# Optimization experiments

Hardware: AMD Instinct MI355X
Metric: run time of the kernel (lower is better)

Reference implementation:

```python
import jax, jax.numpy as jnp
import numpy as np

B, N, D = 8, 4096, 256
H = 8
DH = D // H          # 32 per-head dim
M = 256              # number of random features
DEPTH = 4
HID = 4 * D          # mlp hidden
EPS = 1e-6


def layernorm(x, g, b):
    mu = jnp.mean(x, axis=-1, keepdims=True)
    var = jnp.mean(jnp.square(x - mu), axis=-1, keepdims=True)
    return (x - mu) * jax.lax.rsqrt(var + EPS) * g + b


def _phi(t, proj, is_query):
    # t: (B,H,N,DH), proj: (M,DH) -> (B,H,N,M) nonnegative softmax-kernel features
    nrm = DH ** -0.25
    td = t * nrm
    u = jnp.einsum('bhnd,md->bhnm', td, proj)
    diag = 0.5 * jnp.sum(td * td, axis=-1, keepdims=True)
    if is_query:
        mx = jnp.max(u, axis=-1, keepdims=True)
    else:
        mx = jnp.max(u, axis=(-2, -1), keepdims=True)
    return (jnp.exp(u - diag - mx) + 1e-4) / jnp.sqrt(jnp.asarray(M, t.dtype))


def performer_attn(h, Wqkv, Wproj, bproj, proj):
    # h: (B,N,D)
    qkv = h @ Wqkv                                   # (B,N,3D)
    q, k, v = jnp.split(qkv, 3, axis=-1)
    to_heads = lambda t: t.reshape(B, N, H, DH).transpose(0, 2, 1, 3)
    q, k, v = to_heads(q), to_heads(k), to_heads(v)  # (B,H,N,DH)
    qp = _phi(q, proj, True)                         # (B,H,N,M)
    kp = _phi(k, proj, False)                        # (B,H,N,M)
    kv = jnp.einsum('bhnm,bhnd->bhmd', kp, v)        # (B,H,M,DH) linear-time context
    z = 1.0 / (jnp.einsum('bhnm,bhm->bhn', qp, kp.sum(axis=2)) + 1e-6)
    out = jnp.einsum('bhnm,bhmd->bhnd', qp, kv) * z[..., None]
    out = out.transpose(0, 2, 1, 3).reshape(B, N, D)
    return out @ Wproj + bproj


def mlp(h, W1, b1, W2, b2):
    return jax.nn.gelu(h @ W1 + b1, approximate=False) @ W2 + b2


def setup_inputs() -> dict:
    key = jax.random.key(0)
    ks = jax.random.split(key, 10)
    inp = {
        'x': jax.random.normal(ks[0], (B, N, D), jnp.float32),
        'pos_emb': 0.02 * jax.random.normal(ks[1], (N, D), jnp.float32),
        'g1n': jnp.ones((D,), jnp.float32),
        'b1n': jnp.zeros((D,), jnp.float32),
        'g2n': jnp.ones((D,), jnp.float32),
        'b2n': jnp.zeros((D,), jnp.float32),
        'Wqkv': 0.02 * jax.random.normal(ks[2], (DEPTH, D, 3 * D), jnp.float32),
        'Wproj': 0.02 * jax.random.normal(ks[3], (DEPTH, D, D), jnp.float32),
        'bproj': jnp.zeros((DEPTH, D), jnp.float32),
        'W1': 0.02 * jax.random.normal(ks[4], (DEPTH, D, HID), jnp.float32),
        'b1m': jnp.zeros((DEPTH, HID), jnp.float32),
        'W2': 0.02 * jax.random.normal(ks[5], (DEPTH, HID, D), jnp.float32),
        'b2m': jnp.zeros((DEPTH, D), jnp.float32),
        'proj_mat': jax.random.normal(ks[6], (DEPTH, M, DH), jnp.float32),
    }
    return inp


def reference(x, pos_emb, g1n, b1n, g2n, b2n, Wqkv, Wproj, bproj, W1, b1m, W2, b2m, proj_mat):
    h = x + pos_emb[None]
    for l in range(DEPTH):  # small fixed depth
        h = h + performer_attn(layernorm(h, g1n, b1n), Wqkv[l], Wproj[l], bproj[l], proj_mat[l])
        h = h + mlp(layernorm(h, g2n, b2n), W1[l], b1m[l], W2[l], b2m[l])
    return h
```

## Files before the change

### kernel.cpp

```cpp
#include <hip/hip_runtime.h>
#include <hip/hip_bf16.h>
#include <math.h>

#define B 8
#define N 4096
#define D 256
#define H 8
#define DH 32
#define M 256
#define DEPTH 4
#define HID 1024
#define NRM 0.4204482076268573f

typedef __attribute__((ext_vector_type(8))) short short8;
typedef __attribute__((ext_vector_type(4))) float f32x4;

static __device__ __forceinline__ unsigned short f2bf(float f) {
    __hip_bfloat16 h = __float2bfloat16(f);
    return __builtin_bit_cast(unsigned short, h);
}
static __device__ __forceinline__ float bfu2f(unsigned short u) {
    unsigned int x = ((unsigned int)u) << 16;
    return __builtin_bit_cast(float, x);
}

__global__ void add_pos_kernel(const float* __restrict__ x, const float* __restrict__ pos,
                               float* __restrict__ h) {
    int i = blockIdx.x * 256 + threadIdx.x;
    int nd = i % (N * D);
    h[i] = x[i] + pos[nd];
}

__global__ void projbf_kernel(const float* __restrict__ in, unsigned short* __restrict__ out) {
    int i = blockIdx.x * 256 + threadIdx.x;
    out[i] = f2bf(in[i]);
}

__global__ __launch_bounds__(256) void wtrans_kernel(const float* __restrict__ in,
                                                     unsigned short* __restrict__ out,
                                                     int Kd, int Nd, int slim) {
    __shared__ float tl[32][33];
    int n0 = blockIdx.x * 32, k0 = blockIdx.y * 32;
    int t = threadIdx.x;
    int kk = t >> 3, c4 = (t & 7) * 4;
    float4 v = *reinterpret_cast<const float4*>(&in[(size_t)(k0 + kk) * Nd + n0 + c4]);
    tl[kk][c4 + 0] = v.x; tl[kk][c4 + 1] = v.y; tl[kk][c4 + 2] = v.z; tl[kk][c4 + 3] = v.w;
    __syncthreads();
    int nn = t >> 3, k4 = (t & 7) * 4;
    float sc = (n0 + nn < slim) ? NRM : 1.0f;
    ushort4 o;
    o.x = f2bf(tl[k4 + 0][nn] * sc); o.y = f2bf(tl[k4 + 1][nn] * sc);
    o.z = f2bf(tl[k4 + 2][nn] * sc); o.w = f2bf(tl[k4 + 3][nn] * sc);
    *reinterpret_cast<ushort4*>(&out[(size_t)(n0 + nn) * Kd + k0 + k4]) = o;
}

__global__ __launch_bounds__(256) void ln_kernel(const float* __restrict__ in,
                                                 const float* __restrict__ g,
                                                 const float* __restrict__ bb,
                                                 unsigned short* __restrict__ out) {
    int wave = threadIdx.x >> 6, lane = threadIdx.x & 63;
    long row = (long)blockIdx.x * 4 + wave;
    float4 v = reinterpret_cast<const float4*>(in + row * D)[lane];
    float s = v.x + v.y + v.z + v.w;
#pragma unroll
    for (int o = 32; o >= 1; o >>= 1) s += __shfl_xor(s, o);
    float mu = s * (1.0f / D);
    float d0 = v.x - mu, d1 = v.y - mu, d2 = v.z - mu, d3 = v.w - mu;
    float ss = d0 * d0 + d1 * d1 + d2 * d2 + d3 * d3;
#pragma unroll
    for (int o = 32; o >= 1; o >>= 1) ss += __shfl_xor(ss, o);
    float inv = rsqrtf(ss * (1.0f / D) + 1e-6f);
    float4 gv = reinterpret_cast<const float4*>(g)[lane];
    float4 bv = reinterpret_cast<const float4*>(bb)[lane];
    ushort4 o4;
    o4.x = f2bf(d0 * inv * gv.x + bv.x);
    o4.y = f2bf(d1 * inv * gv.y + bv.y);
    o4.z = f2bf(d2 * inv * gv.z + bv.z);
    o4.w = f2bf(d3 * inv * gv.w + bv.w);
    *reinterpret_cast<ushort4*>(&out[row * D + lane * 4]) = o4;
}

template <bool BIAS, bool GELU_ACT, bool RESID, bool OUT16>
__global__ __launch_bounds__(256) void mgemm_kernel(const unsigned short* __restrict__ A,
                                                    const unsigned short* __restrict__ Bt,
                                                    const float* __restrict__ bias,
                                                    float* __restrict__ C,
                                                    unsigned short* __restrict__ O16,
                                                    int K, int Nc) {
    __shared__ short Als[128][40];
    __shared__ short Bls[128][40];
    int t = threadIdx.x;
    int l = t & 63, w = t >> 6;
    int wr = w >> 1, wc = w & 1;
    int nwg = gridDim.x * gridDim.y;
    int bid = blockIdx.y * gridDim.x + blockIdx.x;
    int lgid = (bid & 7) * (nwg >> 3) + (bid >> 3);
    int bx = lgid % gridDim.x;
    int by = lgid / gridDim.x;
    long m0 = (long)by * 128;
    int n0 = bx * 128;
    int lr = l & 15;
    int lg = l >> 4;
    int kp8 = lg * 8;
    int srow = t >> 2, skoff = (t & 3) * 8;

    const unsigned short* Ap0 = &A[(size_t)(m0 + srow) * K + skoff];
    const unsigned short* Ap1 = Ap0 + (size_t)64 * K;
    const unsigned short* Bp0 = &Bt[(size_t)(n0 + srow) * K + skoff];
    const unsigned short* Bp1 = Bp0 + (size_t)64 * K;

    short8 ra0 = *reinterpret_cast<const short8*>(Ap0);
    short8 ra1 = *reinterpret_cast<const short8*>(Ap1);
    short8 rb0 = *reinterpret_cast<const short8*>(Bp0);
    short8 rb1 = *reinterpret_cast<const short8*>(Bp1);

    f32x4 acc[4][4];
#pragma unroll
    for (int i = 0; i < 4; i++)
#pragma unroll
        for (int j = 0; j < 4; j++) acc[i][j] = (f32x4){0.f, 0.f, 0.f, 0.f};

    for (int k0 = 0; k0 < K; k0 += 32) {
        *reinterpret_cast<short8*>(&Als[srow][skoff]) = ra0;
        *reinterpret_cast<short8*>(&Als[srow + 64][skoff]) = ra1;
        *reinterpret_cast<short8*>(&Bls[srow][skoff]) = rb0;
        *reinterpret_cast<short8*>(&Bls[srow + 64][skoff]) = rb1;
        __syncthreads();
        if (k0 + 32 < K) {
            ra0 = *reinterpret_cast<const short8*>(Ap0 + k0 + 32);
            ra1 = *reinterpret_cast<const short8*>(Ap1 + k0 + 32);
            rb0 = *reinterpret_cast<const short8*>(Bp0 + k0 + 32);
            rb1 = *reinterpret_cast<const short8*>(Bp1 + k0 + 32);
        }
        short8 a[4], b[4];
#pragma unroll
        for (int i = 0; i < 4; i++)
            a[i] = *reinterpret_cast<const short8*>(&Als[wr * 64 + i * 16 + lr][kp8]);
#pragma unroll
        for (int j = 0; j < 4; j++)
            b[j] = *reinterpret_cast<const short8*>(&Bls[wc * 64 + j * 16 + lr][kp8]);
#pragma unroll
        for (int i = 0; i < 4; i++)
#pragma unroll
            for (int j = 0; j < 4; j++)
                acc[i][j] = __builtin_amdgcn_mfma_f32_16x16x32_bf16(b[j], a[i], acc[i][j], 0, 0, 0);
        __syncthreads();
    }

    float4 bias4[4];
    if (BIAS) {
#pragma unroll
        for (int j = 0; j < 4; j++)
            bias4[j] = *reinterpret_cast<const float4*>(&bias[n0 + wc * 64 + j * 16 + lg * 4]);
    }
#pragma unroll
    for (int i = 0; i < 4; i++) {
        long grow = m0 + wr * 64 + i * 16 + lr;
#pragma unroll
        for (int j = 0; j < 4; j++) {
            int gcol = n0 + wc * 64 + j * 16 + lg * 4;
            f32x4 v = acc[i][j];
            if (BIAS) {
                v[0] += bias4[j].x; v[1] += bias4[j].y; v[2] += bias4[j].z; v[3] += bias4[j].w;
            }
            if (GELU_ACT) {
#pragma unroll
                for (int r = 0; r < 4; r++)
                    v[r] = 0.5f * v[r] * (1.0f + erff(v[r] * 0.70710678118654752f));
            }
            if (OUT16) {
                short4 o;
                o.x = (short)f2bf(v[0]); o.y = (short)f2bf(v[1]);
                o.z = (short)f2bf(v[2]); o.w = (short)f2bf(v[3]);
                *reinterpret_cast<short4*>(&O16[grow * Nc + gcol]) = o;
            } else if (RESID) {
                float4 c0 = *reinterpret_cast<const float4*>(&C[grow * Nc + gcol]);
                c0.x += v[0]; c0.y += v[1]; c0.z += v[2]; c0.w += v[3];
                *reinterpret_cast<float4*>(&C[grow * Nc + gcol]) = c0;
            } else {
                float4 c0 = {v[0], v[1], v[2], v[3]};
                *reinterpret_cast<float4*>(&C[grow * Nc + gcol]) = c0;
            }
        }
    }
}

#define KV_P 16
#define KV_ROWS (N / KV_P)
#define PSZ 8484
__global__ __launch_bounds__(256) void kv_kernel(const unsigned short* __restrict__ qkv16,
                                                 const unsigned short* __restrict__ projbf,
                                                 float* __restrict__ kvp) {
    __shared__ __align__(16) unsigned short kp_s[256][64];
    __shared__ __align__(16) unsigned short vT_s[32][66];
    __shared__ float red[4];
    __shared__ float asumred[4][256];
    __shared__ float vred[256][4];
    int t = threadIdx.x;
    int l = t & 63, w = t >> 6;
    int lr = l & 15, lg = l >> 4;
    int bh = blockIdx.x, b = bh >> 3, h = bh & 7;
    int n0 = blockIdx.y * KV_ROWS;
    int rsw = (lr & 7) << 3;

    f32x4 kvacc[4][2];
#pragma unroll
    for (int mf = 0; mf < 4; mf++)
#pragma unroll
        for (int dd = 0; dd < 2; dd++) kvacc[mf][dd] = (f32x4){0.f, 0.f, 0.f, 0.f};
    float asum_p[16];
#pragma unroll
    for (int f = 0; f < 16; f++) asum_p[f] = 0.f;
    float4 vs4 = {0.f, 0.f, 0.f, 0.f};
    float cmax = -1e30f;

    for (int c = 0; c < KV_ROWS / 64; c++) {
        __syncthreads();
        size_t kbase = ((size_t)(b * N) + n0 + c * 64 + w * 16 + lr) * 768 + 256 + h * 32 + lg * 8;
        short8 aq = *reinterpret_cast<const short8*>(qkv16 + kbase);
        float sq = 0.f;
#pragma unroll
        for (int e = 0; e < 8; e++) {
            float xx = bfu2f((unsigned short)aq[e]);
            sq += xx * xx;
        }
        sq += __shfl_xor(sq, 16);
        sq += __shfl_xor(sq, 32);
        float dgr[4];
#pragma unroll
        for (int r = 0; r < 4; r++) dgr[r] = 0.5f * __shfl(sq, lg * 4 + r);
        int cbase = (w * 16 + lg * 4) ^ rsw;
#pragma unroll
        for (int f = 0; f < 16; f++) {
            short8 bq = *reinterpret_cast<const short8*>(projbf + (f * 16 + lr) * 32 + lg * 8);
            f32x4 u = __builtin_amdgcn_mfma_f32_16x16x32_bf16(aq, bq, (f32x4){0.f, 0.f, 0.f, 0.f}, 0, 0, 0);
            cmax = fmaxf(cmax, fmaxf(fmaxf(u[0], u[1]), fmaxf(u[2], u[3])));
            float p0 = __expf(u[0] - dgr[0]);
            float p1 = __expf(u[1] - dgr[1]);
            float p2 = __expf(u[2] - dgr[2]);
            float p3 = __expf(u[3] - dgr[3]);
            asum_p[f] += p0 + p1 + p2 + p3;
            short4 o;
            o.x = (short)f2bf(p0); o.y = (short)f2bf(p1);
            o.z = (short)f2bf(p2); o.w = (short)f2bf(p3);
            *reinterpret_cast<short4*>(&kp_s[f * 16 + lr][cbase]) = o;
        }
#pragma unroll
        for (int ii = 0; ii < 2; ii++) {
            int idx = t + ii * 256;
            int nn = idx >> 3, dz = (idx & 7) * 4;
            const unsigned short* vp =
                qkv16 + ((size_t)(b * N) + n0 + c * 64 + nn) * 768 + 512 + h * 32 + dz;
            short4 vv = *reinterpret_cast<const short4*>(vp);
            float v0 = bfu2f((unsigned short)vv.x), v1 = bfu2f((unsigned short)vv.y);
            float v2 = bfu2f((unsigned short)vv.z), v3 = bfu2f((unsigned short)vv.w);
            vs4.x += v0; vs4.y += v1; vs4.z += v2; vs4.w += v3;
            vT_s[dz + 0][nn] = (unsigned short)vv.x; vT_s[dz + 1][nn] = (unsigned short)vv.y;
            vT_s[dz + 2][nn] = (unsigned short)vv.z; vT_s[dz + 3][nn] = (unsigned short)vv.w;
        }
        __syncthreads();
#pragma unroll
        for (int ks = 0; ks < 2; ks++) {
            short8 bv0 = *reinterpret_cast<const short8*>(&vT_s[lr][ks * 32 + lg * 8]);
            short8 bv1 = *reinterpret_cast<const short8*>(&vT_s[16 + lr][ks * 32 + lg * 8]);
#pragma unroll
            for (int mf = 0; mf < 4; mf++) {
                short8 am = *reinterpret_cast<const short8*>(
                    &kp_s[w * 64 + mf * 16 + lr][(ks * 32 + lg * 8) ^ rsw]);
                kvacc[mf][0] = __builtin_amdgcn_mfma_f32_16x16x32_bf16(am, bv0, kvacc[mf][0], 0, 0, 0);
                kvacc[mf][1] = __builtin_amdgcn_mfma_f32_16x16x32_bf16(am, bv1, kvacc[mf][1], 0, 0, 0);
            }
        }
    }
#pragma unroll
    for (int f = 0; f < 16; f++) {
        asum_p[f] += __shfl_xor(asum_p[f], 16);
        asum_p[f] += __shfl_xor(asum_p[f], 32);
    }
    if (l < 16) {
#pragma unroll
        for (int f = 0; f < 16; f++) asumred[w][f * 16 + l] = asum_p[f];
    }
    vred[t][0] = vs4.x; vred[t][1] = vs4.y; vred[t][2] = vs4.z; vred[t][3] = vs4.w;
#pragma unroll
    for (int o = 1; o < 64; o <<= 1) cmax = fmaxf(cmax, __shfl_xor(cmax, o));
    if (l == 0) red[w] = cmax;
    __syncthreads();
    size_t base = ((size_t)bh * KV_P + blockIdx.y) * PSZ;
#pragma unroll
    for (int mf = 0; mf < 4; mf++)
#pragma unroll
        for (int dd = 0; dd < 2; dd++) {
            int m = w * 64 + mf * 16 + lg * 4;
            int d = dd * 16 + lr;
            float4 o;
            o.x = kvacc[mf][dd][0]; o.y = kvacc[mf][dd][1];
            o.z = kvacc[mf][dd][2]; o.w = kvacc[mf][dd][3];
            *reinterpret_cast<float4*>(&kvp[base + (size_t)d * 256 + m]) = o;
        }
    {
        float s = asumred[0][t] + asumred[1][t] + asumred[2][t] + asumred[3][t];
        kvp[base + 8192 + t] = s;
    }
    if (t < 32) {
        int f4g = t >> 2, cc = t & 3;
        float s = 0.f;
#pragma unroll
        for (int g = 0; g < 32; g++) s += vred[g * 8 + f4g][cc];
        kvp[base + 8448 + t] = s;
    }
    if (t == 0) kvp[base + 8480] = fmaxf(fmaxf(red[0], red[1]), fmaxf(red[2], red[3]));
}

__global__ __launch_bounds__(256) void kv_combine_kernel(const float* __restrict__ kvp,
                                                         unsigned short* __restrict__ kvTb,
                                                         float* __restrict__ ksumf) {
    __shared__ float vst[32];
    int t = threadIdx.x;
    int bh = blockIdx.x >> 2, dq = blockIdx.x & 3;
    size_t base0 = (size_t)bh * KV_P * PSZ;
    float gm = -1e30f;
#pragma unroll
    for (int p = 0; p < KV_P; p++) gm = fmaxf(gm, kvp[base0 + p * PSZ + 8480]);
    if (t < 32) {
        float s = 0.f;
#pragma unroll
        for (int p = 0; p < KV_P; p++) s += kvp[base0 + p * PSZ + 8448 + t];
        vst[t] = s;
    }
    __syncthreads();
    float es = __expf(-gm);
    int d = dq * 8 + (t >> 5);
    int m0 = (t & 31) * 8;
    float4 a0 = {0.f, 0.f, 0.f, 0.f}, a1 = {0.f, 0.f, 0.f, 0.f};
#pragma unroll
    for (int p = 0; p < KV_P; p++) {
        const float* src = &kvp[base0 + p * PSZ + (size_t)d * 256 + m0];
        float4 x0 = *reinterpret_cast<const float4*>(src);
        float4 x1 = *reinterpret_cast<const float4*>(src + 4);
        a0.x += x0.x; a0.y += x0.y; a0.z += x0.z; a0.w += x0.w;
        a1.x += x1.x; a1.y += x1.y; a1.z += x1.z; a1.w += x1.w;
    }
    float vadd = 1e-4f * vst[d];
    ushort4 o0, o1;
    o0.x = f2bf((a0.x * es + vadd) * 0.0625f); o0.y = f2bf((a0.y * es + vadd) * 0.0625f);
    o0.z = f2bf((a0.z * es + vadd) * 0.0625f); o0.w = f2bf((a0.w * es + vadd) * 0.0625f);
    o1.x = f2bf((a1.x * es + vadd) * 0.0625f); o1.y = f2bf((a1.y * es + vadd) * 0.0625f);
    o1.z = f2bf((a1.z * es + vadd) * 0.0625f); o1.w = f2bf((a1.w * es + vadd) * 0.0625f);
    *reinterpret_cast<ushort4*>(&kvTb[((size_t)bh * 32 + d) * 256 + m0]) = o0;
    *reinterpret_cast<ushort4*>(&kvTb[((size_t)bh * 32 + d) * 256 + m0 + 4]) = o1;
    if (dq == 0) {
        float S = 0.f;
#pragma unroll
        for (int p = 0; p < KV_P; p++) S += kvp[base0 + p * PSZ + 8192 + t];
        ksumf[bh * 256 + t] = (S * es + 1e-4f * (float)N) * 0.0625f;
    }
}

#define ATT_TILES 8
__global__ __launch_bounds__(256) void attn_kernel(const unsigned short* __restrict__ qkv16,
                                                   const unsigned short* __restrict__ projbf,
                                                   const unsigned short* __restrict__ kvTb,
                                                   const float* __restrict__ ksumf,
                                                   unsigned short* __restrict__ attn16) {
    __shared__ __align__(16) unsigned short qp_s[64 * 256];
    int t = threadIdx.x;
    int l = t & 63, w = t >> 6;
    int lr = l & 15, lg = l >> 4;
    int bh = blockIdx.x, b = bh >> 3, h = bh & 7;
    int swz = (lr & 7) << 3;
    int row = w * 16 + lr;

    const unsigned short* kvb = kvTb + (size_t)bh * 32 * 256;
    short8 kva0[8], kva1[8];
#pragma unroll
    for (int k0 = 0; k0 < 8; k0++) {
        kva0[k0] = *reinterpret_cast<const short8*>(kvb + (size_t)lr * 256 + k0 * 32 + lg * 8);
        kva1[k0] = *reinterpret_cast<const short8*>(kvb + (size_t)(16 + lr) * 256 + k0 * 32 + lg * 8);
    }

    int tile0 = blockIdx.y * ATT_TILES;
    size_t qstep = (size_t)64 * 768;
    size_t qbase = ((size_t)(b * N) + tile0 * 64 + w * 16 + lr) * 768 + h * 32 + lg * 8;
    short8 qf = *reinterpret_cast<const short8*>(qkv16 + qbase);

    for (int tl = 0; tl < ATT_TILES; tl++) {
        short8 qfn = qf;
        if (tl < ATT_TILES - 1)
            qfn = *reinterpret_cast<const short8*>(qkv16 + qbase + (size_t)(tl + 1) * qstep);

        float sq = 0.f;
#pragma unroll
        for (int e = 0; e < 8; e++) {
            float xx = bfu2f((unsigned short)qf[e]);
            sq += xx * xx;
        }
        sq += __shfl_xor(sq, 16);
        sq += __shfl_xor(sq, 32);
        float dg = 0.5f * sq;

        f32x4 ua[16];
#pragma unroll
        for (int f = 0; f < 16; f++) {
            short8 bq = *reinterpret_cast<const short8*>(projbf + (f * 16 + lr) * 32 + lg * 8);
            ua[f] = __builtin_amdgcn_mfma_f32_16x16x32_bf16(bq, qf, (f32x4){0.f, 0.f, 0.f, 0.f}, 0, 0, 0);
        }

        float mx = -1e30f;
#pragma unroll
        for (int f = 0; f < 16; f++)
#pragma unroll
            for (int r = 0; r < 4; r++) mx = fmaxf(mx, ua[f][r]);
        mx = fmaxf(mx, __shfl_xor(mx, 16));
        mx = fmaxf(mx, __shfl_xor(mx, 32));

        float zs = 0.f;
#pragma unroll
        for (int f = 0; f < 16; f++) {
            float4 ks4 = *reinterpret_cast<const float4*>(&ksumf[bh * 256 + f * 16 + lg * 4]);
            float p0 = (__expf(ua[f][0] - dg - mx) + 1e-4f) * 0.0625f;
            float p1 = (__expf(ua[f][1] - dg - mx) + 1e-4f) * 0.0625f;
            float p2 = (__expf(ua[f][2] - dg - mx) + 1e-4f) * 0.0625f;
            float p3 = (__expf(ua[f][3] - dg - mx) + 1e-4f) * 0.0625f;
            zs += p0 * ks4.x + p1 * ks4.y + p2 * ks4.z + p3 * ks4.w;
            short4 o;
            o.x = (short)f2bf(p0); o.y = (short)f2bf(p1);
            o.z = (short)f2bf(p2); o.w = (short)f2bf(p3);
            *reinterpret_cast<short4*>(&qp_s[row * 256 + ((f * 16 + lg * 4) ^ swz)]) = o;
        }
        zs += __shfl_xor(zs, 16);
        zs += __shfl_xor(zs, 32);
        float zf = 1.0f / (zs + 1e-6f);

        f32x4 oacc[2];
        oacc[0] = (f32x4){0.f, 0.f, 0.f, 0.f};
        oacc[1] = (f32x4){0.f, 0.f, 0.f, 0.f};
#pragma unroll
        for (int k0 = 0; k0 < 8; k0++) {
            short8 qpf = *reinterpret_cast<const short8*>(
                &qp_s[row * 256 + ((k0 * 32 + lg * 8) ^ swz)]);
            oacc[0] = __builtin_amdgcn_mfma_f32_16x16x32_bf16(kva0[k0], qpf, oacc[0], 0, 0, 0);
            oacc[1] = __builtin_amdgcn_mfma_f32_16x16x32_bf16(kva1[k0], qpf, oacc[1], 0, 0, 0);
        }
        size_t orow = ((size_t)(b * N) + (tile0 + tl) * 64 + w * 16 + lr) * 256 + h * 32;
#pragma unroll
        for (int dd = 0; dd < 2; dd++) {
            short4 o;
            o.x = (short)f2bf(oacc[dd][0] * zf);
            o.y = (short)f2bf(oacc[dd][1] * zf);
            o.z = (short)f2bf(oacc[dd][2] * zf);
            o.w = (short)f2bf(oacc[dd][3] * zf);
            *reinterpret_cast<short4*>(&attn16[orow + dd * 16 + lg * 4]) = o;
        }
        qf = qfn;
    }
}

extern "C" void kernel_launch(void* const* d_in, const int* in_sizes, int n_in,
                              void* d_out, int out_size, void* d_ws, size_t ws_size,
                              hipStream_t stream) {
    const float* x = (const float*)d_in[0];
    const float* pos = (const float*)d_in[1];
    const float* g1 = (const float*)d_in[2];
    const float* b1 = (const float*)d_in[3];
    const float* g2 = (const float*)d_in[4];
    const float* b2 = (const float*)d_in[5];
    const float* Wqkv = (const float*)d_in[6];
    const float* Wproj = (const float*)d_in[7];
    const float* bproj = (const float*)d_in[8];
    const float* W1 = (const float*)d_in[9];
    const float* b1m = (const float*)d_in[10];
    const float* W2 = (const float*)d_in[11];
    const float* b2m = (const float*)d_in[12];
    const float* projm = (const float*)d_in[13];

    float* h = (float*)d_out;
    char* p = (char*)d_ws;
    auto alloc = [&](size_t bytes) { char* r = p; p += (bytes + 255) & ~(size_t)255; return r; };
    unsigned short* wbf    = (unsigned short*)alloc((size_t)DEPTH * 786432 * 2);
    unsigned short* projb  = (unsigned short*)alloc((size_t)DEPTH * M * DH * 2);
    unsigned short* ln16   = (unsigned short*)alloc((size_t)B * N * D * 2);
    unsigned short* qkv16  = (unsigned short*)alloc((size_t)B * N * HID * 2);
    unsigned short* hid16  = qkv16;
    unsigned short* attn16 = (unsigned short*)alloc((size_t)B * N * D * 2);
    float* kvp             = (float*)alloc((size_t)64 * KV_P * PSZ * 4);
    unsigned short* kvTb   = (unsigned short*)alloc((size_t)64 * 32 * 256 * 2);
    float* ksumf           = (float*)alloc((size_t)64 * 256 * 4);

    for (int l = 0; l < DEPTH; l++) {
        size_t lb = (size_t)l * 786432;
        wtrans_kernel<<<dim3(768 / 32, 256 / 32), 256, 0, stream>>>(
            Wqkv + (size_t)l * D * 3 * D, wbf + lb + 0, 256, 768, 512);
        wtrans_kernel<<<dim3(256 / 32, 256 / 32), 256, 0, stream>>>(
            Wproj + (size_t)l * D * D, wbf + lb + 196608, 256, 256, 0);
        wtrans_kernel<<<dim3(1024 / 32, 256 / 32), 256, 0, stream>>>(
            W1 + (size_t)l * D * HID, wbf + lb + 262144, 256, 1024, 0);
        wtrans_kernel<<<dim3(256 / 32, 1024 / 32), 256, 0, stream>>>(
            W2 + (size_t)l * HID * D, wbf + lb + 524288, 1024, 256, 0);
    }
    projbf_kernel<<<DEPTH * M * DH / 256, 256, 0, stream>>>(projm, projb);

    add_pos_kernel<<<B * N * D / 256, 256, 0, stream>>>(x, pos, h);

    for (int l = 0; l < DEPTH; l++) {
        size_t lb = (size_t)l * 786432;
        const unsigned short* wqT = wbf + lb + 0;
        const unsigned short* wpT = wbf + lb + 196608;
        const unsigned short* w1T = wbf + lb + 262144;
        const unsigned short* w2T = wbf + lb + 524288;
        const float* bp = bproj + (size_t)l * D;
        const float* b1l = b1m + (size_t)l * HID;
        const float* b2l = b2m + (size_t)l * D;
        const unsigned short* prb = projb + (size_t)l * M * DH;

        ln_kernel<<<B * N / 4, 256, 0, stream>>>(h, g1, b1, ln16);
        mgemm_kernel<false, false, false, true><<<dim3(768 / 128, B * N / 128), 256, 0, stream>>>(
            ln16, wqT, nullptr, nullptr, qkv16, 256, 768);
        kv_kernel<<<dim3(B * H, KV_P), 256, 0, stream>>>(qkv16, prb, kvp);
        kv_combine_kernel<<<B * H * 4, 256, 0, stream>>>(kvp, kvTb, ksumf);
        attn_kernel<<<dim3(B * H, (N / 64) / ATT_TILES), 256, 0, stream>>>(
            qkv16, prb, kvTb, ksumf, attn16);
        mgemm_kernel<true, false, true, false><<<dim3(256 / 128, B * N / 128), 256, 0, stream>>>(
            attn16, wpT, bp, h, nullptr, 256, 256);
        ln_kernel<<<B * N / 4, 256, 0, stream>>>(h, g2, b2, ln16);
        mgemm_kernel<true, true, false, true><<<dim3(1024 / 128, B * N / 128), 256, 0, stream>>>(
            ln16, w1T, b1l, nullptr, hid16, 256, 1024);
        mgemm_kernel<true, false, true, false><<<dim3(256 / 128, B * N / 128), 256, 0, stream>>>(
            hid16, w2T, b2l, h, nullptr, 1024, 256);
    }
}
```

Before: 913.3 us.

## Load GEMM MFMA fragments directly from global memory, dropping LDS staging

The tiled bf16 GEMM no longer stages A and B tiles through shared memory. Each wave now loads its MFMA operand fragments straight from global memory into registers and prefetches the next K-slice. This removes LDS writes, LDS reads and both block barriers per K step. In exchange, each A/B row is fetched separately by the two waves that share it, which doubles global/L2 traffic, and the per-lane 16-byte loads are strided by K, so coalescing is worse.

```diff
diff --git a/kernel.cpp b/kernel.cpp
--- a/kernel.cpp
+++ b/kernel.cpp
@@ -87,8 +87,6 @@
                                                     float* __restrict__ C,
                                                     unsigned short* __restrict__ O16,
                                                     int K, int Nc) {
-    __shared__ short Als[128][40];
-    __shared__ short Bls[128][40];
     int t = threadIdx.x;
     int l = t & 63, w = t >> 6;
     int wr = w >> 1, wc = w & 1;
@@ -102,17 +100,21 @@
     int lr = l & 15;
     int lg = l >> 4;
     int kp8 = lg * 8;
-    int srow = t >> 2, skoff = (t & 3) * 8;
-
-    const unsigned short* Ap0 = &A[(size_t)(m0 + srow) * K + skoff];
-    const unsigned short* Ap1 = Ap0 + (size_t)64 * K;
-    const unsigned short* Bp0 = &Bt[(size_t)(n0 + srow) * K + skoff];
-    const unsigned short* Bp1 = Bp0 + (size_t)64 * K;
-
-    short8 ra0 = *reinterpret_cast<const short8*>(Ap0);
-    short8 ra1 = *reinterpret_cast<const short8*>(Ap1);
-    short8 rb0 = *reinterpret_cast<const short8*>(Bp0);
-    short8 rb1 = *reinterpret_cast<const short8*>(Bp1);
+
+    const unsigned short* Ap[4];
+    const unsigned short* Bp[4];
+#pragma unroll
+    for (int i = 0; i < 4; i++) {
+        Ap[i] = A + (size_t)(m0 + wr * 64 + i * 16 + lr) * K + kp8;
+        Bp[i] = Bt + (size_t)(n0 + wc * 64 + i * 16 + lr) * K + kp8;
+    }
+
+    short8 ca[4], cb[4];
+#pragma unroll
+    for (int i = 0; i < 4; i++) {
+        ca[i] = *reinterpret_cast<const short8*>(Ap[i]);
+        cb[i] = *reinterpret_cast<const short8*>(Bp[i]);
+    }
 
     f32x4 acc[4][4];
 #pragma unroll
@@ -121,30 +123,23 @@
         for (int j = 0; j < 4; j++) acc[i][j] = (f32x4){0.f, 0.f, 0.f, 0.f};
 
     for (int k0 = 0; k0 < K; k0 += 32) {
-        *reinterpret_cast<short8*>(&Als[srow][skoff]) = ra0;
-        *reinterpret_cast<short8*>(&Als[srow + 64][skoff]) = ra1;
-        *reinterpret_cast<short8*>(&Bls[srow][skoff]) = rb0;
-        *reinterpret_cast<short8*>(&Bls[srow + 64][skoff]) = rb1;
-        __syncthreads();
+        short8 na[4], nb[4];
         if (k0 + 32 < K) {
-            ra0 = *reinterpret_cast<const short8*>(Ap0 + k0 + 32);
-            ra1 = *reinterpret_cast<const short8*>(Ap1 + k0 + 32);
-            rb0 = *reinterpret_cast<const short8*>(Bp0 + k0 + 32);
-            rb1 = *reinterpret_cast<const short8*>(Bp1 + k0 + 32);
-        }
-        short8 a[4], b[4];
+#pragma unroll
+            for (int i = 0; i < 4; i++) {
+                na[i] = *reinterpret_cast<const short8*>(Ap[i] + k0 + 32);
+                nb[i] = *reinterpret_cast<const short8*>(Bp[i] + k0 + 32);
+            }
+        }
 #pragma unroll
         for (int i = 0; i < 4; i++)
-            a[i] = *reinterpret_cast<const short8*>(&Als[wr * 64 + i * 16 + lr][kp8]);
-#pragma unroll
-        for (int j = 0; j < 4; j++)
-            b[j] = *reinterpret_cast<const short8*>(&Bls[wc * 64 + j * 16 + lr][kp8]);
-#pragma unroll
-        for (int i = 0; i < 4; i++)
 #pragma unroll
             for (int j = 0; j < 4; j++)
-                acc[i][j] = __builtin_amdgcn_mfma_f32_16x16x32_bf16(b[j], a[i], acc[i][j], 0, 0, 0);
-        __syncthreads();
+                acc[i][j] = __builtin_amdgcn_mfma_f32_16x16x32_bf16(cb[j], ca[i], acc[i][j], 0, 0, 0);
+        if (k0 + 32 < K) {
+#pragma unroll
+            for (int i = 0; i < 4; i++) { ca[i] = na[i]; cb[i] = nb[i]; }
+        }
     }
 
     float4 bias4[4];
```

Result: slower. 1.330 ms (+45.7%).

## Use direct global-to-LDS loads with XOR-swizzled unpadded tiles in GEMM

Applied to the files above, without the earlier changes.

Replaces the register-staged global loads and LDS stores in the bf16 MFMA GEMM with global_load_lds 16-byte direct copies into shared memory. Padding is removed and an XOR swizzle on the k-chunk index is used on both the write and read sides to avoid LDS bank conflicts. This cuts VGPR use and LDS store instructions, but drops the register prefetch of the next tile, so global latency is no longer overlapped with compute within a block.

```diff
diff --git a/kernel.cpp b/kernel.cpp
--- a/kernel.cpp
+++ b/kernel.cpp
@@ -22,6 +22,11 @@
 static __device__ __forceinline__ float bfu2f(unsigned short u) {
     unsigned int x = ((unsigned int)u) << 16;
     return __builtin_bit_cast(float, x);
+}
+static __device__ __forceinline__ void gload16(const void* g, void* l) {
+    __builtin_amdgcn_global_load_lds(
+        (const __attribute__((address_space(1))) void*)g,
+        (__attribute__((address_space(3))) void*)l, 16, 0, 0);
 }
 
 __global__ void add_pos_kernel(const float* __restrict__ x, const float* __restrict__ pos,
@@ -87,8 +92,8 @@
                                                     float* __restrict__ C,
                                                     unsigned short* __restrict__ O16,
                                                     int K, int Nc) {
-    __shared__ short Als[128][40];
-    __shared__ short Bls[128][40];
+    __shared__ __align__(16) short Als[128][32];
+    __shared__ __align__(16) short Bls[128][32];
     int t = threadIdx.x;
     int l = t & 63, w = t >> 6;
     int wr = w >> 1, wc = w & 1;
@@ -101,18 +106,18 @@
     int n0 = bx * 128;
     int lr = l & 15;
     int lg = l >> 4;
-    int kp8 = lg * 8;
-    int srow = t >> 2, skoff = (t & 3) * 8;
-
-    const unsigned short* Ap0 = &A[(size_t)(m0 + srow) * K + skoff];
-    const unsigned short* Ap1 = Ap0 + (size_t)64 * K;
-    const unsigned short* Bp0 = &Bt[(size_t)(n0 + srow) * K + skoff];
-    const unsigned short* Bp1 = Bp0 + (size_t)64 * K;
-
-    short8 ra0 = *reinterpret_cast<const short8*>(Ap0);
-    short8 ra1 = *reinterpret_cast<const short8*>(Ap1);
-    short8 rb0 = *reinterpret_cast<const short8*>(Bp0);
-    short8 rb1 = *reinterpret_cast<const short8*>(Bp1);
+    int srow = t >> 2;
+    int skoff = (((t & 3) ^ ((srow >> 1) & 3))) * 8;
+    int cswz = (lg ^ ((lr >> 1) & 3)) * 8;
+
+    short* aw0 = &Als[w * 16][0];
+    short* aw1 = &Als[w * 16 + 64][0];
+    short* bw0 = &Bls[w * 16][0];
+    short* bw1 = &Bls[w * 16 + 64][0];
+    const unsigned short* Asrc0 = &A[(size_t)(m0 + srow) * K + skoff];
+    const unsigned short* Asrc1 = Asrc0 + (size_t)64 * K;
+    const unsigned short* Bsrc0 = &Bt[(size_t)(n0 + srow) * K + skoff];
+    const unsigned short* Bsrc1 = Bsrc0 + (size_t)64 * K;
 
     f32x4 acc[4][4];
 #pragma unroll
@@ -121,24 +126,18 @@
         for (int j = 0; j < 4; j++) acc[i][j] = (f32x4){0.f, 0.f, 0.f, 0.f};
 
     for (int k0 = 0; k0 < K; k0 += 32) {
-        *reinterpret_cast<short8*>(&Als[srow][skoff]) = ra0;
-        *reinterpret_cast<short8*>(&Als[srow + 64][skoff]) = ra1;
-        *reinterpret_cast<short8*>(&Bls[srow][skoff]) = rb0;
-        *reinterpret_cast<short8*>(&Bls[srow + 64][skoff]) = rb1;
+        gload16(Asrc0 + k0, aw0);
+        gload16(Asrc1 + k0, aw1);
+        gload16(Bsrc0 + k0, bw0);
+        gload16(Bsrc1 + k0, bw1);
         __syncthreads();
-        if (k0 + 32 < K) {
-            ra0 = *reinterpret_cast<const short8*>(Ap0 + k0 + 32);
-            ra1 = *reinterpret_cast<const short8*>(Ap1 + k0 + 32);
-            rb0 = *reinterpret_cast<const short8*>(Bp0 + k0 + 32);
-            rb1 = *reinterpret_cast<const short8*>(Bp1 + k0 + 32);
-        }
         short8 a[4], b[4];
 #pragma unroll
         for (int i = 0; i < 4; i++)
-            a[i] = *reinterpret_cast<const short8*>(&Als[wr * 64 + i * 16 + lr][kp8]);
+            a[i] = *reinterpret_cast<const short8*>(&Als[wr * 64 + i * 16 + lr][cswz]);
 #pragma unroll
         for (int j = 0; j < 4; j++)
-            b[j] = *reinterpret_cast<const short8*>(&Bls[wc * 64 + j * 16 + lr][kp8]);
+            b[j] = *reinterpret_cast<const short8*>(&Bls[wc * 64 + j * 16 + lr][cswz]);
 #pragma unroll
         for (int i = 0; i < 4; i++)
 #pragma unroll
```

New measurement: 941.1 us. 3.0% more time.

## Double-buffer and swizzle LDS in MFMA GEMM, use tanh GELU

Applied to the files above, without the earlier changes.

The bf16 MFMA GEMM now uses two LDS buffers: the next tile is written while the current one is read, and one barrier per k-step is removed. Padding is replaced with an XOR column swizzle to avoid bank conflicts while halving padding waste. The exact erf GELU epilogue is replaced by the tanh approximation using a fast exp. This adds small numerical deviation from the exact GELU the reference specifies.

```diff
diff --git a/kernel.cpp b/kernel.cpp
--- a/kernel.cpp
+++ b/kernel.cpp
@@ -22,6 +22,12 @@
 static __device__ __forceinline__ float bfu2f(unsigned short u) {
     unsigned int x = ((unsigned int)u) << 16;
     return __builtin_bit_cast(float, x);
+}
+static __device__ __forceinline__ float gelu_fast(float x) {
+    float z = 0.7978845608028654f * (x + 0.044715f * x * x * x);
+    float e = __expf(2.0f * z);
+    float th = 1.0f - 2.0f / (e + 1.0f);
+    return 0.5f * x * (1.0f + th);
 }
 
 __global__ void add_pos_kernel(const float* __restrict__ x, const float* __restrict__ pos,
@@ -87,8 +93,8 @@
                                                     float* __restrict__ C,
                                                     unsigned short* __restrict__ O16,
                                                     int K, int Nc) {
-    __shared__ short Als[128][40];
-    __shared__ short Bls[128][40];
+    __shared__ __align__(16) short Als[2][128][32];
+    __shared__ __align__(16) short Bls[2][128][32];
     int t = threadIdx.x;
     int l = t & 63, w = t >> 6;
     int wr = w >> 1, wc = w & 1;
@@ -101,8 +107,10 @@
     int n0 = bx * 128;
     int lr = l & 15;
     int lg = l >> 4;
-    int kp8 = lg * 8;
-    int srow = t >> 2, skoff = (t & 3) * 8;
+    int srow = t >> 2, c4 = t & 3;
+    int skoff = c4 * 8;
+    int wcol = (c4 ^ ((srow >> 1) & 3)) * 8;
+    int cswz = (lg ^ ((lr >> 1) & 3)) * 8;
 
     const unsigned short* Ap0 = &A[(size_t)(m0 + srow) * K + skoff];
     const unsigned short* Ap1 = Ap0 + (size_t)64 * K;
@@ -113,6 +121,15 @@
     short8 ra1 = *reinterpret_cast<const short8*>(Ap1);
     short8 rb0 = *reinterpret_cast<const short8*>(Bp0);
     short8 rb1 = *reinterpret_cast<const short8*>(Bp1);
+    *reinterpret_cast<short8*>(&Als[0][srow][wcol]) = ra0;
+    *reinterpret_cast<short8*>(&Als[0][srow + 64][wcol]) = ra1;
+    *reinterpret_cast<short8*>(&Bls[0][srow][wcol]) = rb0;
+    *reinterpret_cast<short8*>(&Bls[0][srow + 64][wcol]) = rb1;
+    ra0 = *reinterpret_cast<const short8*>(Ap0 + 32);
+    ra1 = *reinterpret_cast<const short8*>(Ap1 + 32);
+    rb0 = *reinterpret_cast<const short8*>(Bp0 + 32);
+    rb1 = *reinterpret_cast<const short8*>(Bp1 + 32);
+    __syncthreads();
 
     f32x4 acc[4][4];
 #pragma unroll
@@ -120,25 +137,31 @@
 #pragma unroll
         for (int j = 0; j < 4; j++) acc[i][j] = (f32x4){0.f, 0.f, 0.f, 0.f};
 
-    for (int k0 = 0; k0 < K; k0 += 32) {
-        *reinterpret_cast<short8*>(&Als[srow][skoff]) = ra0;
-        *reinterpret_cast<short8*>(&Als[srow + 64][skoff]) = ra1;
-        *reinterpret_cast<short8*>(&Bls[srow][skoff]) = rb0;
-        *reinterpret_cast<short8*>(&Bls[srow + 64][skoff]) = rb1;
-        __syncthreads();
-        if (k0 + 32 < K) {
-            ra0 = *reinterpret_cast<const short8*>(Ap0 + k0 + 32);
-            ra1 = *reinterpret_cast<const short8*>(Ap1 + k0 + 32);
-            rb0 = *reinterpret_cast<const short8*>(Bp0 + k0 + 32);
-            rb1 = *reinterpret_cast<const short8*>(Bp1 + k0 + 32);
-        }
+    int nk = K >> 5;
+#pragma unroll 2
+    for (int it = 0; it < nk; it++) {
+        int buf = it & 1;
         short8 a[4], b[4];
 #pragma unroll
         for (int i = 0; i < 4; i++)
-            a[i] = *reinterpret_cast<const short8*>(&Als[wr * 64 + i * 16 + lr][kp8]);
+            a[i] = *reinterpret_cast<const short8*>(&Als[buf][wr * 64 + i * 16 + lr][cswz]);
 #pragma unroll
         for (int j = 0; j < 4; j++)
-            b[j] = *reinterpret_cast<const short8*>(&Bls[wc * 64 + j * 16 + lr][kp8]);
+            b[j] = *reinterpret_cast<const short8*>(&Bls[buf][wc * 64 + j * 16 + lr][cswz]);
+        if (it + 1 < nk) {
+            int nb = buf ^ 1;
+            *reinterpret_cast<short8*>(&Als[nb][srow][wcol]) = ra0;
+            *reinterpret_cast<short8*>(&Als[nb][srow + 64][wcol]) = ra1;
+            *reinterpret_cast<short8*>(&Bls[nb][srow][wcol]) = rb0;
+            *reinterpret_cast<short8*>(&Bls[nb][srow + 64][wcol]) = rb1;
+            if (it + 2 < nk) {
+                int ko = (it + 2) * 32;
+                ra0 = *reinterpret_cast<const short8*>(Ap0 + ko);
+                ra1 = *reinterpret_cast<const short8*>(Ap1 + ko);
+                rb0 = *reinterpret_cast<const short8*>(Bp0 + ko);
+                rb1 = *reinterpret_cast<const short8*>(Bp1 + ko);
+            }
+        }
 #pragma unroll
         for (int i = 0; i < 4; i++)
 #pragma unroll
@@ -165,8 +188,7 @@
             }
             if (GELU_ACT) {
 #pragma unroll
-                for (int r = 0; r < 4; r++)
-                    v[r] = 0.5f * v[r] * (1.0f + erff(v[r] * 0.70710678118654752f));
+                for (int r = 0; r < 4; r++) v[r] = gelu_fast(v[r]);
             }
             if (OUT16) {
                 short4 o;
```

Result: no change. 907.7 us (-0.6%).
